# Performance work log

Hardware: AMD Instinct MI355X
Metric: run time of the kernel (lower is better)

Reference implementation:

```python
import jax, jax.numpy as jnp
import numpy as np

PAD_IDX = 0
VOCAB = 60
HIDDEN = 128
BATCH = 1024
SEQ = 256


def setup_inputs() -> dict:
    key = jax.random.key(0)
    ks = jax.random.split(key, 6)
    x = jax.random.randint(ks[0], (BATCH, SEQ), 0, VOCAB, dtype=jnp.int64 if jax.config.jax_enable_x64 else jnp.int32)
    lengths = jax.random.randint(ks[1], (BATCH,), 1, SEQ + 1, dtype=x.dtype)
    emb = jax.random.normal(ks[2], (VOCAB, HIDDEN), dtype=jnp.float32) * 0.1
    emb = emb.at[PAD_IDX].set(0.0)  # nn.Embedding padding_idx row is zero
    W_ih = jax.random.normal(ks[3], (HIDDEN, HIDDEN), dtype=jnp.float32) * (1.0 / np.sqrt(HIDDEN))
    W_hh = jax.random.normal(ks[4], (HIDDEN, HIDDEN), dtype=jnp.float32) * (1.0 / np.sqrt(HIDDEN))
    W_fc = jax.random.normal(ks[5], (VOCAB, HIDDEN), dtype=jnp.float32) * (1.0 / np.sqrt(HIDDEN))
    b_fc = jnp.zeros((VOCAB,), dtype=jnp.float32)
    return {"x": x, "lengths": lengths, "emb": emb, "W_ih": W_ih,
            "W_hh": W_hh, "W_fc": W_fc, "b_fc": b_fc}


def reference(x, lengths, emb, W_ih, W_hh, W_fc, b_fc):
    embedded = emb[x]                      # [B, T, H]
    B = embedded.shape[0]
    h0 = jnp.zeros((B, HIDDEN), dtype=embedded.dtype)

    def step(h_prev, x_t):
        # z_t = x_t @ W_ih^T + h_prev @ W_hh^T ; h_t = tanh(z_t)
        h_t = jnp.tanh(x_t @ W_ih.T + h_prev @ W_hh.T)
        return h_t, h_t

    _, hs = jax.lax.scan(step, h0, jnp.swapaxes(embedded, 0, 1))  # hs: [T, B, H]
    outputs = jnp.swapaxes(hs, 0, 1)       # [B, T, H]
    last_out = jnp.take_along_axis(outputs, (lengths - 1)[:, None, None], axis=1)[:, 0, :]  # [B, H]
    return last_out @ W_fc.T + b_fc[None, :]
```

## Files before the change

kernel.cpp:

```cpp
#include <hip/hip_runtime.h>
#include <hip/hip_bf16.h>

#define BATCH 1024
#define SEQ 256
#define HIDDEN 128
#define VOCAB 60
#define ROWS 4
#define ASTRIDE 136
#define EWSTRIDE 132

typedef _Float16 f16x8 __attribute__((ext_vector_type(8)));
typedef _Float16 f16x4 __attribute__((ext_vector_type(4)));
typedef float f32x4 __attribute__((ext_vector_type(4)));

__device__ __forceinline__ float fast_tanh(float x) {
    float e = __builtin_amdgcn_exp2f(x * 2.8853900817779268f);
    return __builtin_fmaf(-2.0f, __builtin_amdgcn_rcpf(e + 1.0f), 1.0f);
}

__global__ void rnn_prep_embw(const float* __restrict__ emb,
                              const float* __restrict__ W_ih,
                              float* __restrict__ embW) {
    const int v = blockIdx.x;
    const int i = threadIdx.x;
    __shared__ __align__(16) float e[HIDDEN];
    e[i] = emb[v * HIDDEN + i];
    __syncthreads();
    const float4* wrow = (const float4*)(W_ih + i * HIDDEN);
    const float4* e4 = (const float4*)e;
    float a0 = 0.f, a1 = 0.f, a2 = 0.f, a3 = 0.f;
#pragma unroll
    for (int j = 0; j < HIDDEN / 4; ++j) {
        float4 w = wrow[j];
        float4 h = e4[j];
        a0 += w.x * h.x; a1 += w.y * h.y; a2 += w.z * h.z; a3 += w.w * h.w;
    }
    embW[v * HIDDEN + i] = (a0 + a1) + (a2 + a3);
}

__global__ void __launch_bounds__(512)
rnn_mfma(const int* __restrict__ x, const int* __restrict__ lengths,
         const float* __restrict__ embW, const float* __restrict__ W_hh,
         const float* __restrict__ W_fc, const float* __restrict__ b_fc,
         float* __restrict__ out) {
    const int tid = threadIdx.x;
    const int wave = tid >> 6;
    const int lane = tid & 63;
    const int q = lane >> 4;
    const int r16 = lane & 15;
    const int r4 = r16 & 3;
    const int c0 = wave * 16;
    const int b0 = blockIdx.x * ROWS;

    __shared__ __align__(16) _Float16 Ah[2][ROWS][ASTRIDE];
    __shared__ __align__(16) _Float16 ew[VOCAB][EWSTRIDE];
    __shared__ int xs[ROWS][SEQ + 1];
    __shared__ __align__(16) float hfin[ROWS][HIDDEN];
    __shared__ int lenbuf[ROWS];

    for (int idx = tid; idx < VOCAB * HIDDEN; idx += 512) {
        int v = idx >> 7, c = idx & 127;
        ew[v][c] = (_Float16)embW[idx];
    }
    for (int idx = tid; idx < ROWS * SEQ; idx += 512) {
        int r = idx >> 8, t = idx & (SEQ - 1);
        xs[r][t] = x[(b0 + r) * SEQ + t];
    }
    if (tid < ROWS) lenbuf[tid] = lengths[b0 + tid];
    for (int idx = tid; idx < (int)(sizeof(Ah) / 4); idx += 512)
        ((int*)Ah)[idx] = 0;

    f16x8 Wf[4];
    {
        const float* wrow = W_hh + (c0 + r16) * HIDDEN + q * 8;
#pragma unroll
        for (int kc = 0; kc < 4; ++kc) {
            const float* p = wrow + kc * 32;
#pragma unroll
            for (int j = 0; j < 8; ++j) Wf[kc][j] = (_Float16)p[j];
        }
    }

    __syncthreads();

    const int mylen = lenbuf[r4];
    int lenmax = 0;
#pragma unroll
    for (int r = 0; r < ROWS; ++r) lenmax = max(lenmax, lenbuf[r]);

    int tok = xs[r4][0];
    f16x4 sd = *(const f16x4*)&ew[tok][c0 + 4 * q];
    int tok1 = xs[r4][1];

    int cur = 0;
    f32x4 cap = {0.f, 0.f, 0.f, 0.f};

    for (int t = 0; t < lenmax; ++t) {
        const _Float16* hb = &Ah[cur][r4][q * 8];
        f16x8 H0 = *(const f16x8*)(hb + 0);
        f16x8 H1 = *(const f16x8*)(hb + 32);
        f16x8 H2 = *(const f16x8*)(hb + 64);
        f16x8 H3 = *(const f16x8*)(hb + 96);

        f16x4 sn = *(const f16x4*)&ew[tok1][c0 + 4 * q];
        const int t2 = (t + 2 < SEQ) ? t + 2 : SEQ - 1;
        const int tok2 = xs[r4][t2];

        f32x4 a = {(float)sd[0], (float)sd[1], (float)sd[2], (float)sd[3]};
        f32x4 d = {0.f, 0.f, 0.f, 0.f};
        a = __builtin_amdgcn_mfma_f32_16x16x32_f16(Wf[0], H0, a, 0, 0, 0);
        d = __builtin_amdgcn_mfma_f32_16x16x32_f16(Wf[2], H2, d, 0, 0, 0);
        a = __builtin_amdgcn_mfma_f32_16x16x32_f16(Wf[1], H1, a, 0, 0, 0);
        d = __builtin_amdgcn_mfma_f32_16x16x32_f16(Wf[3], H3, d, 0, 0, 0);
        f32x4 z = a + d;

        f32x4 th;
        th[0] = fast_tanh(z[0]);
        th[1] = fast_tanh(z[1]);
        th[2] = fast_tanh(z[2]);
        th[3] = fast_tanh(z[3]);
        if (t + 1 == mylen) cap = th;

        uint2 pk;
        pk.x = __builtin_bit_cast(unsigned int, __builtin_amdgcn_cvt_pkrtz(th[0], th[1]));
        pk.y = __builtin_bit_cast(unsigned int, __builtin_amdgcn_cvt_pkrtz(th[2], th[3]));

        const int nxt = cur ^ 1;
        if (r16 < ROWS)
            *(uint2*)&Ah[nxt][r16][c0 + 4 * q] = pk;
        __syncthreads();
        cur = nxt;
        sd = sn;
        tok1 = tok2;
    }

    if (r16 < ROWS)
        *(f32x4*)&hfin[r16][c0 + 4 * q] = cap;
    __syncthreads();

    const int r = tid >> 7;
    const int c = tid & 127;
    if (c < VOCAB) {
        const float4* hv = (const float4*)hfin[r];
        const float4* wf = (const float4*)(W_fc + c * HIDDEN);
        float a0 = 0.f, a1 = 0.f, a2 = 0.f, a3 = 0.f;
#pragma unroll
        for (int j = 0; j < HIDDEN / 4; ++j) {
            float4 h = hv[j];
            float4 w = wf[j];
            a0 += h.x * w.x; a1 += h.y * w.y; a2 += h.z * w.z; a3 += h.w * w.w;
        }
        out[(b0 + r) * VOCAB + c] = (a0 + a1) + (a2 + a3) + b_fc[c];
    }
}

extern "C" void kernel_launch(void* const* d_in, const int* in_sizes, int n_in,
                              void* d_out, int out_size, void* d_ws, size_t ws_size,
                              hipStream_t stream) {
    const int* x = (const int*)d_in[0];
    const int* lengths = (const int*)d_in[1];
    const float* emb = (const float*)d_in[2];
    const float* W_ih = (const float*)d_in[3];
    const float* W_hh = (const float*)d_in[4];
    const float* W_fc = (const float*)d_in[5];
    const float* b_fc = (const float*)d_in[6];
    float* out = (float*)d_out;

    float* embW = (float*)d_ws;

    rnn_prep_embw<<<VOCAB, HIDDEN, 0, stream>>>(emb, W_ih, embW);
    rnn_mfma<<<BATCH / ROWS, 512, 0, stream>>>(x, lengths, embW, W_hh, W_fc, b_fc, out);
}
```

Before: 173.7 us.

## Stage per-chunk input projections in an fp32 LDS ring instead of an fp16 table

Drops the whole-vocabulary fp16 embW table from shared memory. Every 16 timesteps the block gathers fp32 projected embeddings for the next chunk from global memory into an LDS ring, and each step reads its bias term from there. This removes the dependent token-to-table lookup from the serial step loop and keeps the input term in fp32. The cost is one extra barrier per chunk plus a global gather that is not overlapped with the recurrence, and the ring uses more LDS.

```diff
diff --git a/kernel.cpp b/kernel.cpp
--- a/kernel.cpp
+++ b/kernel.cpp
@@ -6,8 +6,9 @@
 #define HIDDEN 128
 #define VOCAB 60
 #define ROWS 4
-#define ASTRIDE 136
-#define EWSTRIDE 132
+#define CHUNK 16
+#define ASTRIDE 144
+#define RSTR 136
 
 typedef _Float16 f16x8 __attribute__((ext_vector_type(8)));
 typedef _Float16 f16x4 __attribute__((ext_vector_type(4)));
@@ -52,16 +53,12 @@
     const int c0 = wave * 16;
     const int b0 = blockIdx.x * ROWS;
 
+    __shared__ __align__(16) float ring[CHUNK][ROWS][RSTR];
     __shared__ __align__(16) _Float16 Ah[2][ROWS][ASTRIDE];
-    __shared__ __align__(16) _Float16 ew[VOCAB][EWSTRIDE];
     __shared__ int xs[ROWS][SEQ + 1];
     __shared__ __align__(16) float hfin[ROWS][HIDDEN];
     __shared__ int lenbuf[ROWS];
 
-    for (int idx = tid; idx < VOCAB * HIDDEN; idx += 512) {
-        int v = idx >> 7, c = idx & 127;
-        ew[v][c] = (_Float16)embW[idx];
-    }
     for (int idx = tid; idx < ROWS * SEQ; idx += 512) {
         int r = idx >> 8, t = idx & (SEQ - 1);
         xs[r][t] = x[(b0 + r) * SEQ + t];
@@ -88,50 +85,55 @@
 #pragma unroll
     for (int r = 0; r < ROWS; ++r) lenmax = max(lenmax, lenbuf[r]);
 
-    int tok = xs[r4][0];
-    f16x4 sd = *(const f16x4*)&ew[tok][c0 + 4 * q];
-    int tok1 = xs[r4][1];
-
     int cur = 0;
     f32x4 cap = {0.f, 0.f, 0.f, 0.f};
 
-    for (int t = 0; t < lenmax; ++t) {
-        const _Float16* hb = &Ah[cur][r4][q * 8];
-        f16x8 H0 = *(const f16x8*)(hb + 0);
-        f16x8 H1 = *(const f16x8*)(hb + 32);
-        f16x8 H2 = *(const f16x8*)(hb + 64);
-        f16x8 H3 = *(const f16x8*)(hb + 96);
+    for (int t0 = 0; t0 < lenmax; t0 += CHUNK) {
+#pragma unroll
+        for (int k = 0; k < 4; ++k) {
+            int idx = tid + k * 512;
+            int c4 = idx & 31;
+            int r = (idx >> 5) & 3;
+            int tp = idx >> 7;
+            int tok = xs[r][t0 + tp];
+            f32x4 v = *(const f32x4*)(embW + tok * HIDDEN + c4 * 4);
+            *(f32x4*)&ring[tp][r][c4 * 4] = v;
+        }
+        __syncthreads();
 
-        f16x4 sn = *(const f16x4*)&ew[tok1][c0 + 4 * q];
-        const int t2 = (t + 2 < SEQ) ? t + 2 : SEQ - 1;
-        const int tok2 = xs[r4][t2];
+        const int tend = (lenmax - t0 < CHUNK) ? lenmax - t0 : CHUNK;
+        for (int tt = 0; tt < tend; ++tt) {
+            const _Float16* hb = &Ah[cur][r4][q * 8];
+            f16x8 H0 = *(const f16x8*)(hb + 0);
+            f16x8 H1 = *(const f16x8*)(hb + 32);
+            f16x8 H2 = *(const f16x8*)(hb + 64);
+            f16x8 H3 = *(const f16x8*)(hb + 96);
 
-        f32x4 a = {(float)sd[0], (float)sd[1], (float)sd[2], (float)sd[3]};
-        f32x4 d = {0.f, 0.f, 0.f, 0.f};
-        a = __builtin_amdgcn_mfma_f32_16x16x32_f16(Wf[0], H0, a, 0, 0, 0);
-        d = __builtin_amdgcn_mfma_f32_16x16x32_f16(Wf[2], H2, d, 0, 0, 0);
-        a = __builtin_amdgcn_mfma_f32_16x16x32_f16(Wf[1], H1, a, 0, 0, 0);
-        d = __builtin_amdgcn_mfma_f32_16x16x32_f16(Wf[3], H3, d, 0, 0, 0);
-        f32x4 z = a + d;
+            f32x4 a = *(const f32x4*)&ring[tt][r4][c0 + 4 * q];
+            f32x4 d = {0.f, 0.f, 0.f, 0.f};
+            a = __builtin_amdgcn_mfma_f32_16x16x32_f16(Wf[0], H0, a, 0, 0, 0);
+            d = __builtin_amdgcn_mfma_f32_16x16x32_f16(Wf[2], H2, d, 0, 0, 0);
+            a = __builtin_amdgcn_mfma_f32_16x16x32_f16(Wf[1], H1, a, 0, 0, 0);
+            d = __builtin_amdgcn_mfma_f32_16x16x32_f16(Wf[3], H3, d, 0, 0, 0);
+            f32x4 z = a + d;
 
-        f32x4 th;
-        th[0] = fast_tanh(z[0]);
-        th[1] = fast_tanh(z[1]);
-        th[2] = fast_tanh(z[2]);
-        th[3] = fast_tanh(z[3]);
-        if (t + 1 == mylen) cap = th;
+            f32x4 th;
+            th[0] = fast_tanh(z[0]);
+            th[1] = fast_tanh(z[1]);
+            th[2] = fast_tanh(z[2]);
+            th[3] = fast_tanh(z[3]);
+            if (t0 + tt + 1 == mylen) cap = th;
 
-        uint2 pk;
-        pk.x = __builtin_bit_cast(unsigned int, __builtin_amdgcn_cvt_pkrtz(th[0], th[1]));
-        pk.y = __builtin_bit_cast(unsigned int, __builtin_amdgcn_cvt_pkrtz(th[2], th[3]));
+            uint2 pk;
+            pk.x = __builtin_bit_cast(unsigned int, __builtin_amdgcn_cvt_pkrtz(th[0], th[1]));
+            pk.y = __builtin_bit_cast(unsigned int, __builtin_amdgcn_cvt_pkrtz(th[2], th[3]));
 
-        const int nxt = cur ^ 1;
-        if (r16 < ROWS)
-            *(uint2*)&Ah[nxt][r16][c0 + 4 * q] = pk;
-        __syncthreads();
-        cur = nxt;
-        sd = sn;
-        tok1 = tok2;
+            const int nxt = cur ^ 1;
+            if (r16 < ROWS)
+                *(uint2*)&Ah[nxt][r16][c0 + 4 * q] = pk;
+            __syncthreads();
+            cur = nxt;
+        }
     }
 
     if (r16 < ROWS)
```

Result: faster. 164.4 us (-5.4%).
